# Kernel optimization log

Hardware: AMD Instinct MI355X
Metric: run time of the kernel (lower is better)

The kernel has to match this reference:

```python
import jax, jax.numpy as jnp
import numpy as np

D_MODEL = 1024
NUM_HEADS = 16
D_K = D_MODEL // NUM_HEADS  # 64
THETA = 10000.0


def setup_inputs() -> dict:
    key = jax.random.key(0)
    k_x, k_q, k_k, k_v, k_o = jax.random.split(key, 5)
    B, S = 2, 2048
    std = (2.0 / (D_MODEL + D_MODEL)) ** 0.5
    x = jax.random.normal(k_x, (B, S, D_MODEL), dtype=jnp.float32)
    Wq = std * jax.random.truncated_normal(k_q, -3.0, 3.0, (D_MODEL, D_MODEL), dtype=jnp.float32)
    Wk = std * jax.random.truncated_normal(k_k, -3.0, 3.0, (D_MODEL, D_MODEL), dtype=jnp.float32)
    Wv = std * jax.random.truncated_normal(k_v, -3.0, 3.0, (D_MODEL, D_MODEL), dtype=jnp.float32)
    Wo = std * jax.random.truncated_normal(k_o, -3.0, 3.0, (D_MODEL, D_MODEL), dtype=jnp.float32)
    return {"x": x, "Wq": Wq, "Wk": Wk, "Wv": Wv, "Wo": Wo}


def _apply_rope(t, cos, sin):
    # t: [B, H, S, d_k]; cos/sin: [S, d_k//2] broadcast over B, H
    tr = t.reshape(*t.shape[:-1], D_K // 2, 2)
    t1, t2 = tr[..., 0], tr[..., 1]
    r1 = t1 * cos - t2 * sin
    r2 = t1 * sin + t2 * cos
    return jnp.stack([r1, r2], axis=-1).reshape(t.shape)


def reference(x, Wq, Wk, Wv, Wo):
    B, S, D = x.shape
    H, dk = NUM_HEADS, D_K
    # projections (no bias): y = x @ W.T
    Q = (x @ Wq.T).reshape(B, S, H, dk).transpose(0, 2, 1, 3)  # [B,H,S,dk]
    K = (x @ Wk.T).reshape(B, S, H, dk).transpose(0, 2, 1, 3)
    V = (x @ Wv.T).reshape(B, S, H, dk).transpose(0, 2, 1, 3)
    # RoPE angles for positions 0..S-1
    pos = jnp.arange(S, dtype=jnp.float32)[:, None]            # [S,1]
    freqs = 1.0 / (THETA ** (jnp.arange(0, dk, 2, dtype=jnp.float32) / dk))  # [dk/2]
    angles = pos * freqs[None, :]                              # [S, dk/2]
    cos, sin = jnp.cos(angles), jnp.sin(angles)
    Q = _apply_rope(Q, cos, sin)
    K = _apply_rope(K, cos, sin)
    # causal scaled dot-product attention
    scores = jnp.einsum("bhqd,bhkd->bhqk", Q, K) / jnp.sqrt(jnp.float32(dk))
    causal = jnp.tril(jnp.ones((S, S), dtype=bool))
    scores = jnp.where(causal, scores, -jnp.inf)
    probs = jax.nn.softmax(scores, axis=-1)
    attn = jnp.einsum("bhqk,bhkd->bhqd", probs, V)             # [B,H,S,dk]
    attn = attn.transpose(0, 2, 1, 3).reshape(B, S, H * dk)
    return attn @ Wo.T
```

## Files before the change

### kernel.cpp

```cpp
#include <hip/hip_runtime.h>
#include <hip/hip_bf16.h>

typedef __bf16 bf16;
typedef __bf16 bf16x8 __attribute__((ext_vector_type(8)));
typedef float f32x4 __attribute__((ext_vector_type(4)));

#define MFMA16(A, B, C) __builtin_amdgcn_mfma_f32_16x16x32_bf16((A), (B), (C), 0, 0, 0)

static __device__ __forceinline__ void gload16(const bf16* g, bf16* l) {
    __builtin_amdgcn_global_load_lds((const __attribute__((address_space(1))) void*)g,
                                     (__attribute__((address_space(3))) void*)l, 16, 0, 0);
}

__global__ void detect_kernel(const void* w, int* flag) {
    float v = (float)((const bf16*)w)[threadIdx.x];
    unsigned long long bad = __ballot(!(fabsf(v) < 1.0f));
    if (threadIdx.x == 0) *flag = bad ? 1 : 0;
}

__global__ __launch_bounds__(256) void convert_all(const void* x, const void* w0,
                                                   const void* w1, const void* w2,
                                                   const void* w3, bf16* xb, bf16* b0,
                                                   bf16* b1, bf16* b2, bf16* b3,
                                                   const int* flagp) {
    if (*flagp == 0) return;
    int id = (blockIdx.x * 256 + threadIdx.x) * 4;
    const int XN = 1 << 22;
    const float* src;
    bf16* dst;
    int off;
    if (id < XN) {
        src = (const float*)x; dst = xb; off = id;
    } else {
        int r = id - XN;
        int wi = r >> 20;
        off = r & ((1 << 20) - 1);
        src = (const float*)(wi == 0 ? w0 : wi == 1 ? w1 : wi == 2 ? w2 : w3);
        dst = (wi == 0 ? b0 : wi == 1 ? b1 : wi == 2 ? b2 : b3);
    }
    float4 v = *(const float4*)(src + off);
    bf16 o[4] = {(bf16)v.x, (bf16)v.y, (bf16)v.z, (bf16)v.w};
    *(uint2*)(dst + off) = *(uint2*)o;
}

template <int MODE>
__global__ __launch_bounds__(128, 3) void gemm_nt(const void* rawA, const bf16* convA,
                                                  const void* rW0, const bf16* cW0,
                                                  const void* rW1, const bf16* cW1,
                                                  const void* rW2, const bf16* cW2,
                                                  bf16* Qo, bf16* Ko, bf16* Vt,
                                                  void* Cout, const int* flagp) {
    const int K = 1024;
    __shared__ __attribute__((aligned(16))) bf16 lsA[2][128 * 32];
    __shared__ __attribute__((aligned(16))) bf16 lsB[2][64 * 32];
    const int flag = *flagp;
    const bf16* A = flag ? convA : (const bf16*)rawA;
    int tensor, n0;
    const bf16* W;
    if (MODE == 0) {
        tensor = blockIdx.x >> 4;
        n0 = (blockIdx.x & 15) * 64;
        W = tensor == 0 ? (flag ? cW0 : (const bf16*)rW0)
          : tensor == 1 ? (flag ? cW1 : (const bf16*)rW1)
                        : (flag ? cW2 : (const bf16*)rW2);
    } else {
        tensor = 0;
        n0 = blockIdx.x * 64;
        W = flag ? cW0 : (const bf16*)rW0;
    }
    const int t = threadIdx.x;
    const int m0 = blockIdx.y * 128;
    const int w = t >> 6, lane = t & 63;
    const int llo = lane & 15, quad = lane >> 4;
    const int sel = (llo >> 1) & 3;

    f32x4 acc[4][4] = {};

    auto stage = [&](int k0, int buf) {
#pragma unroll
        for (int j = 0; j < 4; ++j) {
            int c = j * 128 + t;
            int row = c >> 2, pos = c & 3;
            int g = pos ^ ((row >> 1) & 3);
            gload16(A + (size_t)(m0 + row) * K + k0 + g * 8, &lsA[buf][c * 8]);
        }
#pragma unroll
        for (int j = 0; j < 2; ++j) {
            int c = j * 128 + t;
            int row = c >> 2, pos = c & 3;
            int g = pos ^ ((row >> 1) & 3);
            gload16(W + (size_t)(n0 + row) * K + k0 + g * 8, &lsB[buf][c * 8]);
        }
    };

    auto compute = [&](int buf) {
        bf16x8 a[4], bb[4];
#pragma unroll
        for (int mi = 0; mi < 4; ++mi) {
            int r = w * 64 + mi * 16 + llo;
            a[mi] = *(const bf16x8*)&lsA[buf][r * 32 + ((quad ^ sel) * 8)];
        }
#pragma unroll
        for (int ni = 0; ni < 4; ++ni) {
            int r = ni * 16 + llo;
            bb[ni] = *(const bf16x8*)&lsB[buf][r * 32 + ((quad ^ sel) * 8)];
        }
#pragma unroll
        for (int mi = 0; mi < 4; ++mi)
#pragma unroll
            for (int ni = 0; ni < 4; ++ni)
                acc[mi][ni] = MFMA16(a[mi], bb[ni], acc[mi][ni]);
    };

    stage(0, 0);
    for (int it = 0; it < 32; it += 2) {
        __syncthreads();
        stage((it + 1) * 32, 1);
        compute(0);
        __syncthreads();
        if (it + 2 < 32) stage((it + 2) * 32, 0);
        compute(1);
    }

#pragma unroll
    for (int mi = 0; mi < 4; ++mi)
#pragma unroll
        for (int ni = 0; ni < 4; ++ni)
#pragma unroll
            for (int r = 0; r < 4; ++r) {
                int row = m0 + w * 64 + mi * 16 + quad * 4 + r;
                int col = n0 + ni * 16 + llo;
                float v = acc[mi][ni][r];
                if (MODE == 1) {
                    if (flag)
                        ((float*)Cout)[(size_t)row * 1024 + col] = v;
                    else
                        ((bf16*)Cout)[(size_t)row * 1024 + col] = (bf16)v;
                } else if (tensor == 2) {
                    int b = row >> 11, s = row & 2047;
                    Vt[((size_t)b * 1024 + col) * 2048 + s] = (bf16)v;
                } else {
                    int d = col & 63, s = row & 2047;
                    float partner = __shfl_xor(v, 1);
                    float freq = exp2f((float)(d >> 1) * -0.4152410118609203f);
                    float rev = (float)s * freq * 0.15915494309189535f;
                    rev -= floorf(rev);
                    float sn = __builtin_amdgcn_sinf(rev);
                    float cs = __builtin_amdgcn_cosf(rev);
                    float outv = v * cs + partner * sn * ((d & 1) ? 1.0f : -1.0f);
                    bf16* dst = (tensor == 0) ? Qo : Ko;
                    dst[(size_t)row * 1024 + col] = (bf16)outv;
                }
            }
}

__global__ __launch_bounds__(256, 3) void attn_kernel(const bf16* __restrict__ Q,
                                                      const bf16* __restrict__ Kr,
                                                      const bf16* __restrict__ Vt,
                                                      bf16* __restrict__ O,
                                                      bf16* __restrict__ Opart,
                                                      float* __restrict__ lws) {
    __shared__ __attribute__((aligned(16))) bf16 lsK[2][64 * 64];
    __shared__ __attribute__((aligned(16))) bf16 lsV[2][64 * 64];
    __shared__ __attribute__((aligned(16))) bf16 lsP[4][32 * 64];
    const int blk = blockIdx.x;
    int ib, bh, s, tt0, tt1;
    bool split;
    if (blk < 512) {
        split = true;
        s = blk >> 8;
        int c = blk & 255;
        ib = 15 - (c >> 5);
        bh = c & 31;
        tt0 = s ? (ib + 1) : 0;
        tt1 = s ? (2 * ib + 1) : ib;
    } else {
        split = false;
        s = 0;
        int c = blk - 512;
        ib = c >> 5;
        bh = c & 31;
        tt0 = 0;
        tt1 = 2 * ib + 1;
    }
    const int b = bh >> 4, h = bh & 15;
    const int t = threadIdx.x, w = t >> 6, lane = t & 63;
    const int llo = lane & 15, quad = lane >> 4;
    const int q0w = ib * 128 + w * 32;

    bf16x8 aQ[2][2];
#pragma unroll
    for (int qi = 0; qi < 2; ++qi) {
        const size_t qb =
            ((size_t)(b * 2048 + q0w + qi * 16 + llo)) * 1024 + h * 64 + quad * 8;
        aQ[qi][0] = *(const bf16x8*)&Q[qb];
        aQ[qi][1] = *(const bf16x8*)&Q[qb + 32];
    }

    f32x4 o[2][4] = {};
    float lpart[2] = {0.f, 0.f};
    const float SC = 0.18033688011112042f;
    const int qlane0 = q0w + llo;

    const int srow8 = lane >> 3;
    const int sc = (lane & 7) ^ srow8;

    auto stage = [&](int tt, int buf) {
        const int kv0 = tt * 64;
#pragma unroll
        for (int jj = 0; jj < 2; ++jj) {
            int seg = w + jj * 4;
            int rowk = seg * 8 + srow8;
            gload16(&Kr[((size_t)(b * 2048 + kv0 + rowk)) * 1024 + h * 64 + sc * 8],
                    &lsK[buf][seg * 512 + lane * 8]);
            gload16(&Vt[((size_t)(b * 1024 + h * 64 + rowk)) * 2048 + kv0 + sc * 8],
                    &lsV[buf][seg * 512 + lane * 8]);
        }
    };

    stage(tt0, 0);

    for (int tt = tt0; tt <= tt1; ++tt) {
        const int cur = (tt - tt0) & 1;
        const int kv0 = tt * 64;
        __syncthreads();
        if (tt + 1 <= tt1) stage(tt + 1, cur ^ 1);

        if (kv0 <= q0w + 31) {
            bf16x8 kf[4][2];
#pragma unroll
            for (int half = 0; half < 4; ++half) {
                int rk = half * 16 + llo;
                kf[half][0] = *(const bf16x8*)&lsK[cur][rk * 64 + ((quad ^ (rk & 7)) * 8)];
                kf[half][1] =
                    *(const bf16x8*)&lsK[cur][rk * 64 + (((quad + 4) ^ (rk & 7)) * 8)];
            }
            bf16x8 vf[2][4];
#pragma unroll
            for (int kc = 0; kc < 2; ++kc)
#pragma unroll
                for (int g = 0; g < 4; ++g) {
                    int rv = g * 16 + llo;
                    int cg = kc * 4 + quad;
                    vf[kc][g] =
                        *(const bf16x8*)&lsV[cur][rv * 64 + ((cg ^ (rv & 7)) * 8)];
                }

            const bool need_mask = (kv0 + 63 >= q0w);
#pragma unroll
            for (int qi = 0; qi < 2; ++qi) {
                const int q = qlane0 + qi * 16;
                const int prow = qi * 16 + llo;
#pragma unroll
                for (int half = 0; half < 4; ++half) {
                    f32x4 z = {};
                    z = MFMA16(kf[half][0], aQ[qi][0], z);
                    z = MFMA16(kf[half][1], aQ[qi][1], z);
                    union { bf16 hh[4]; uint2 uu; } pk;
                    if (need_mask) {
                        int kvb = kv0 + half * 16 + quad * 4;
#pragma unroll
                        for (int r = 0; r < 4; ++r) {
                            float e = (kvb + r <= q) ? z[r] * SC : -INFINITY;
                            float p = __builtin_amdgcn_exp2f(e);
                            lpart[qi] += p;
                            pk.hh[r] = (bf16)p;
                        }
                    } else {
#pragma unroll
                        for (int r = 0; r < 4; ++r) {
                            float p = __builtin_amdgcn_exp2f(z[r] * SC);
                            lpart[qi] += p;
                            pk.hh[r] = (bf16)p;
                        }
                    }
                    int cw = 2 * half + (quad >> 1);
                    *(uint2*)&lsP[w][prow * 64 + ((cw ^ (llo & 7)) * 8) + (quad & 1) * 4] =
                        pk.uu;
                }
            }
            __builtin_amdgcn_wave_barrier();
#pragma unroll
            for (int qi = 0; qi < 2; ++qi) {
                const int prow = qi * 16 + llo;
#pragma unroll
                for (int kc = 0; kc < 2; ++kc) {
                    int cr = 4 * kc + quad;
                    bf16x8 aP =
                        *(const bf16x8*)&lsP[w][prow * 64 + ((cr ^ (llo & 7)) * 8)];
#pragma unroll
                    for (int g = 0; g < 4; ++g) o[qi][g] = MFMA16(aP, vf[kc][g], o[qi][g]);
                }
            }
            __builtin_amdgcn_wave_barrier();
        }
    }

    float lfull[2];
#pragma unroll
    for (int qi = 0; qi < 2; ++qi) {
        float l = lpart[qi];
        l += __shfl_xor(l, 16);
        l += __shfl_xor(l, 32);
        lfull[qi] = l;
    }

    if (split) {
        const int slot = ((ib - 8) * 32 + bh) * 2 + s;
        bf16* op = Opart + (size_t)slot * 8192;
#pragma unroll
        for (int qi = 0; qi < 2; ++qi) {
#pragma unroll
            for (int r = 0; r < 4; ++r) {
                int row_in = w * 32 + qi * 16 + quad * 4 + r;
#pragma unroll
                for (int g = 0; g < 4; ++g)
                    op[row_in * 64 + g * 16 + llo] = (bf16)o[qi][g][r];
            }
            if (quad == 0) lws[slot * 128 + w * 32 + qi * 16 + llo] = lfull[qi];
        }
    } else {
#pragma unroll
        for (int qi = 0; qi < 2; ++qi)
#pragma unroll
            for (int r = 0; r < 4; ++r) {
                float l = __shfl(lfull[qi], (lane & 48) | (quad * 4 + r));
                float inv = 1.f / l;
                int q = q0w + qi * 16 + quad * 4 + r;
                size_t ob = ((size_t)(b * 2048 + q)) * 1024 + h * 64;
#pragma unroll
                for (int g = 0; g < 4; ++g)
                    O[ob + g * 16 + llo] = (bf16)(o[qi][g][r] * inv);
            }
    }
}

__global__ __launch_bounds__(256) void combine_kernel(const bf16* __restrict__ Opart,
                                                      const float* __restrict__ lws,
                                                      bf16* __restrict__ AO) {
    int id = blockIdx.x * 256 + threadIdx.x;
    int d = id & 63;
    int h = (id >> 6) & 15;
    int qoff = (id >> 10) & 1023;
    int b = id >> 20;
    int ib8 = qoff >> 7;
    int q_in = qoff & 127;
    int slot = (ib8 * 32 + (b * 16 + h)) * 2;
    size_t base = (size_t)slot * 8192 + q_in * 64 + d;
    float o0 = (float)Opart[base];
    float o1 = (float)Opart[base + 8192];
    float l = lws[slot * 128 + q_in] + lws[(slot + 1) * 128 + q_in];
    int q = 1024 + qoff;
    AO[((size_t)(b * 2048 + q)) * 1024 + h * 64 + d] = (bf16)((o0 + o1) / l);
}

extern "C" void kernel_launch(void* const* d_in, const int* in_sizes, int n_in,
                              void* d_out, int out_size, void* d_ws, size_t ws_size,
                              hipStream_t stream) {
    const size_t TN = (size_t)4096 * 1024;

    int* flag = (int*)d_ws;
    bf16* Q = (bf16*)((char*)d_ws + 256);
    bf16* Kb = Q + TN;
    bf16* Vt = Kb + TN;
    bf16* xb = Vt + TN;
    bf16* Wb0 = xb + TN;
    bf16* Wb1 = Wb0 + TN / 4;
    bf16* Wb2 = Wb1 + TN / 4;
    bf16* Wb3 = Wb2 + TN / 4;
    bf16* AO = Q;
    bf16* Opart = xb;
    float* lws = (float*)Wb0;

    detect_kernel<<<1, 64, 0, stream>>>(d_in[1], flag);
    convert_all<<<8192, 256, 0, stream>>>(d_in[0], d_in[1], d_in[2], d_in[3], d_in[4],
                                          xb, Wb0, Wb1, Wb2, Wb3, flag);

    gemm_nt<0><<<dim3(48, 32), 128, 0, stream>>>(d_in[0], xb, d_in[1], Wb0, d_in[2],
                                                 Wb1, d_in[3], Wb2, Q, Kb, Vt, nullptr,
                                                 flag);

    attn_kernel<<<768, 256, 0, stream>>>(Q, Kb, Vt, AO, Opart, lws);
    combine_kernel<<<8192, 256, 0, stream>>>(Opart, lws, AO);

    gemm_nt<1><<<dim3(16, 32), 128, 0, stream>>>(AO, AO, d_in[4], Wb3, nullptr,
                                                 nullptr, nullptr, nullptr, nullptr,
                                                 nullptr, nullptr, d_out, flag);
}
```

Baseline: 204.7 us.

## Split-K the output projection GEMM with atomic accumulation

Splits the final Wo projection into two K halves, doubling the block count, and accumulates the halves with atomicAdd into a float buffer. Separate kernels zero the accumulation target beforehand and cast to bf16 afterwards when the output is bf16. The aim is to fill the GPU better on a GEMM with few tiles. In exchange it adds atomic traffic, two extra launches and extra memory passes.

```diff
diff --git a/kernel.cpp b/kernel.cpp
--- a/kernel.cpp
+++ b/kernel.cpp
@@ -43,33 +43,56 @@
     *(uint2*)(dst + off) = *(uint2*)o;
 }
 
+__global__ __launch_bounds__(256) void zero_out(float* acc32, float* dout,
+                                                const int* flagp) {
+    int i = (blockIdx.x * 256 + threadIdx.x) * 4;
+    float4 z = {0.f, 0.f, 0.f, 0.f};
+    *(float4*)(acc32 + i) = z;
+    if (*flagp) *(float4*)(dout + i) = z;
+}
+
+__global__ __launch_bounds__(256) void cast_out(const float* acc32, bf16* dout,
+                                                const int* flagp) {
+    if (*flagp) return;
+    int i = (blockIdx.x * 256 + threadIdx.x) * 4;
+    float4 v = *(const float4*)(acc32 + i);
+    bf16 o[4] = {(bf16)v.x, (bf16)v.y, (bf16)v.z, (bf16)v.w};
+    *(uint2*)(dout + i) = *(uint2*)o;
+}
+
 template <int MODE>
 __global__ __launch_bounds__(128, 3) void gemm_nt(const void* rawA, const bf16* convA,
                                                   const void* rW0, const bf16* cW0,
                                                   const void* rW1, const bf16* cW1,
                                                   const void* rW2, const bf16* cW2,
                                                   bf16* Qo, bf16* Ko, bf16* Vt,
-                                                  void* Cout, const int* flagp) {
+                                                  void* Cout, float* accp,
+                                                  const int* flagp) {
     const int K = 1024;
     __shared__ __attribute__((aligned(16))) bf16 lsA[2][128 * 32];
     __shared__ __attribute__((aligned(16))) bf16 lsB[2][64 * 32];
     const int flag = *flagp;
     const bf16* A = flag ? convA : (const bf16*)rawA;
-    int tensor, n0;
+    int tensor, n0, m0, ks;
     const bf16* W;
     if (MODE == 0) {
         tensor = blockIdx.x >> 4;
         n0 = (blockIdx.x & 15) * 64;
+        m0 = blockIdx.y * 128;
+        ks = 0;
         W = tensor == 0 ? (flag ? cW0 : (const bf16*)rW0)
           : tensor == 1 ? (flag ? cW1 : (const bf16*)rW1)
                         : (flag ? cW2 : (const bf16*)rW2);
     } else {
+        const int bid = blockIdx.x;
+        ks = bid & 1;
+        const int slot = bid >> 1;
+        m0 = (slot & 31) * 128;
+        n0 = (slot >> 5) * 64;
         tensor = 0;
-        n0 = blockIdx.x * 64;
         W = flag ? cW0 : (const bf16*)rW0;
     }
     const int t = threadIdx.x;
-    const int m0 = blockIdx.y * 128;
     const int w = t >> 6, lane = t & 63;
     const int llo = lane & 15, quad = lane >> 4;
     const int sel = (llo >> 1) & 3;
@@ -112,13 +135,16 @@
                 acc[mi][ni] = MFMA16(a[mi], bb[ni], acc[mi][ni]);
     };
 
-    stage(0, 0);
-    for (int it = 0; it < 32; it += 2) {
+    const int kbase = (MODE == 1) ? ks * 512 : 0;
+    const int NIT = (MODE == 1) ? 16 : 32;
+
+    stage(kbase, 0);
+    for (int it = 0; it < NIT; it += 2) {
         __syncthreads();
-        stage((it + 1) * 32, 1);
+        stage(kbase + (it + 1) * 32, 1);
         compute(0);
         __syncthreads();
-        if (it + 2 < 32) stage((it + 2) * 32, 0);
+        if (it + 2 < NIT) stage(kbase + (it + 2) * 32, 0);
         compute(1);
     }
 
@@ -132,10 +158,8 @@
                 int col = n0 + ni * 16 + llo;
                 float v = acc[mi][ni][r];
                 if (MODE == 1) {
-                    if (flag)
-                        ((float*)Cout)[(size_t)row * 1024 + col] = v;
-                    else
-                        ((bf16*)Cout)[(size_t)row * 1024 + col] = (bf16)v;
+                    float* dst = flag ? (float*)Cout : accp;
+                    atomicAdd(&dst[(size_t)row * 1024 + col], v);
                 } else if (tensor == 2) {
                     int b = row >> 11, s = row & 2047;
                     Vt[((size_t)b * 1024 + col) * 2048 + s] = (bf16)v;
@@ -306,8 +330,8 @@
     }
 
     if (split) {
-        const int slot = ((ib - 8) * 32 + bh) * 2 + s;
-        bf16* op = Opart + (size_t)slot * 8192;
+        const int slotw = ((ib - 8) * 32 + bh) * 2 + s;
+        bf16* op = Opart + (size_t)slotw * 8192;
 #pragma unroll
         for (int qi = 0; qi < 2; ++qi) {
 #pragma unroll
@@ -317,7 +341,7 @@
                 for (int g = 0; g < 4; ++g)
                     op[row_in * 64 + g * 16 + llo] = (bf16)o[qi][g][r];
             }
-            if (quad == 0) lws[slot * 128 + w * 32 + qi * 16 + llo] = lfull[qi];
+            if (quad == 0) lws[slotw * 128 + w * 32 + qi * 16 + llo] = lfull[qi];
         }
     } else {
 #pragma unroll
@@ -371,6 +395,7 @@
     bf16* AO = Q;
     bf16* Opart = xb;
     float* lws = (float*)Wb0;
+    float* acc32 = (float*)Kb;
 
     detect_kernel<<<1, 64, 0, stream>>>(d_in[1], flag);
     convert_all<<<8192, 256, 0, stream>>>(d_in[0], d_in[1], d_in[2], d_in[3], d_in[4],
@@ -378,12 +403,14 @@
 
     gemm_nt<0><<<dim3(48, 32), 128, 0, stream>>>(d_in[0], xb, d_in[1], Wb0, d_in[2],
                                                  Wb1, d_in[3], Wb2, Q, Kb, Vt, nullptr,
-                                                 flag);
+                                                 nullptr, flag);
 
     attn_kernel<<<768, 256, 0, stream>>>(Q, Kb, Vt, AO, Opart, lws);
     combine_kernel<<<8192, 256, 0, stream>>>(Opart, lws, AO);
 
-    gemm_nt<1><<<dim3(16, 32), 128, 0, stream>>>(AO, AO, d_in[4], Wb3, nullptr,
-                                                 nullptr, nullptr, nullptr, nullptr,
-                                                 nullptr, nullptr, d_out, flag);
-}
+    zero_out<<<4096, 256, 0, stream>>>(acc32, (float*)d_out, flag);
+    gemm_nt<1><<<1024, 128, 0, stream>>>(AO, AO, d_in[4], Wb3, nullptr, nullptr,
+                                         nullptr, nullptr, nullptr, nullptr, nullptr,
+                                         d_out, acc32, flag);
+    cast_out<<<4096, 256, 0, stream>>>(acc32, (bf16*)d_out, flag);
+}
```

Result: slower. 224.3 us (+9.6%).
